# Performance work log

Hardware: AMD Instinct MI355X
Metric: run time of the kernel (lower is better)

## Reference

```python
import jax, jax.numpy as jnp
import numpy as np

N_NODES = 50000
N_EDGES = 600000
IN_FEAT = 128
OUT_FEAT = 128
NUM_RELS = 8


def setup_inputs() -> dict:
    key = jax.random.key(0)
    ks = jax.random.split(key, 8)
    h = jax.random.normal(ks[0], (N_NODES, IN_FEAT), dtype=jnp.float32)
    # xavier_uniform-like scale for relation weights
    limit = float(np.sqrt(6.0 / (IN_FEAT + OUT_FEAT)))
    weight = jax.random.uniform(ks[1], (NUM_RELS, IN_FEAT, OUT_FEAT), jnp.float32, -limit, limit)
    limit_g = float(np.sqrt(6.0 / (IN_FEAT + 1)))
    gate_weight = jax.random.uniform(ks[2], (NUM_RELS, IN_FEAT, 1), jnp.float32, -limit_g, limit_g)
    h_bias = jnp.zeros((OUT_FEAT,), jnp.float32)
    loop_weight = jax.random.uniform(ks[3], (IN_FEAT, OUT_FEAT), jnp.float32, -limit, limit)
    norm = jax.random.uniform(ks[4], (N_EDGES, 1), jnp.float32)
    src = jax.random.randint(ks[5], (N_EDGES,), 0, N_NODES, dtype=jnp.int32)
    dst = jax.random.randint(ks[6], (N_EDGES,), 0, N_NODES, dtype=jnp.int32)
    rel_type = jax.random.randint(ks[7], (N_EDGES,), 0, NUM_RELS, dtype=jnp.int32)
    return {"h": h, "weight": weight, "gate_weight": gate_weight, "h_bias": h_bias,
            "loop_weight": loop_weight, "norm": norm, "src": src, "dst": dst,
            "rel_type": rel_type}


def reference(h, weight, gate_weight, h_bias, loop_weight, norm, src, dst, rel_type):
    n_nodes = h.shape[0]
    # Transform all nodes under every relation once ([R, N, out]); cheaper than
    # materializing per-edge [E, in, out] weight gathers for small R.
    h_rel = jnp.einsum('ni,rio->rno', h, weight)          # [R, N, out]
    msg = h_rel[rel_type, src]                             # [E, out] gather
    msg = msg * norm                                       # per-edge norm
    # relation-specific scalar gate on src features
    gate_rel = jnp.einsum('ni,ri->rn', h, gate_weight[:, :, 0])  # [R, N]
    gate = jax.nn.sigmoid(gate_rel[rel_type, src])[:, None]      # [E, 1]
    msg = msg * gate
    # scatter-sum messages into destination nodes
    agg = jax.ops.segment_sum(msg, dst, num_segments=n_nodes)    # [N, out]
    out = agg + h_bias + h @ loop_weight                   # bias + self-loop
    out = jax.nn.relu(out)                                 # activation
    # dropout p=0.0 (deterministic) -> identity
    return out
```

## Files before the change

### kernel.cpp

```cpp
#include <hip/hip_runtime.h>

#define N_NODES 50000
#define N_EDGES 600000
#define F 128
#define NRELL 9
#define NB_SCAN 196
#define NB2 1563

#define WT3_OFF   0
#define H2_OFF    294912
#define GATE3_OFF 13094912
#define CNT3_OFF  14694912
#define EXCL3_OFF 16294912
#define BSUM3_OFF 17895168
#define REC3_OFF  17901568
#define A3_OFF    22701568
#define WS_NEED3  ((size_t)138012160)

#define GATE_OFF   294912
#define HREL_OFF   1894912
#define HREL_BYTES (9ll*N_NODES*128*2)
#define CNT_OFF    117094912
#define BASE_OFF   117294912
#define CUR_OFF    117494912
#define BSUM_OFF   117694912
#define SORT_OFF   117695936
#define WS_NEED2   ((size_t)120095936)
#define WS_NEED1   ((size_t)HREL_OFF + (size_t)HREL_BYTES)

typedef __attribute__((ext_vector_type(8))) short short8;
typedef __attribute__((ext_vector_type(4))) float floatx4;

__device__ inline unsigned short f32_to_bf16(float f) {
    unsigned u = __float_as_uint(f);
    unsigned r = u + 0x7fff + ((u >> 16) & 1);
    return (unsigned short)(r >> 16);
}
__device__ inline float bf16_to_f32(unsigned short s) {
    return __uint_as_float(((unsigned)s) << 16);
}
__device__ inline float bf16lo(unsigned m) { return __uint_as_float(m << 16); }
__device__ inline float bf16hi(unsigned m) { return __uint_as_float(m & 0xffff0000u); }
__device__ inline float sigmoidf(float x) { return 1.f / (1.f + __expf(-x)); }

__global__ void k_prep_w(const float* __restrict__ W, const float* __restrict__ LW,
                         unsigned short* __restrict__ Wt, int swz) {
    int idx = blockIdx.x * 256 + threadIdx.x;
    if (idx >= 9 * 128 * 128) return;
    int r = idx >> 14;
    int rem = idx & 16383;
    int i = rem >> 7, o = rem & 127;
    float v = (r < 8) ? W[(r << 14) + (i << 7) + o] : LW[(i << 7) + o];
    int pos;
    if (swz) {
        int g = (i >> 3) ^ (o & 7);
        pos = (r << 14) + (o << 7) + (g << 3) + (i & 7);
    } else {
        pos = (r << 14) + (o << 7) + i;
    }
    Wt[pos] = f32_to_bf16(v);
}

__global__ void k_prep_h(const float* __restrict__ h, const float* __restrict__ gw,
                         unsigned short* __restrict__ h2, float* __restrict__ gate) {
    int wave = threadIdx.x >> 6, lane = threadIdx.x & 63;
    int n = blockIdx.x * 4 + wave;
    float2 hv = *(const float2*)(h + (size_t)n * F + lane * 2);
    unsigned val = (unsigned)f32_to_bf16(hv.x) | ((unsigned)f32_to_bf16(hv.y) << 16);
    *(unsigned*)(h2 + (size_t)n * F + lane * 2) = val;
    #pragma unroll
    for (int r = 0; r < 8; ++r) {
        float2 wv = *(const float2*)(gw + r * F + lane * 2);
        float p = hv.x * wv.x + hv.y * wv.y;
        #pragma unroll
        for (int off = 32; off; off >>= 1) p += __shfl_xor(p, off);
        if (lane == 0) gate[r * N_NODES + n] = sigmoidf(p);
    }
}

__global__ void k_hist2(const int* __restrict__ dst, const int* __restrict__ rel,
                        int* __restrict__ cnt) {
    int e = blockIdx.x * 256 + threadIdx.x;
    if (e < N_EDGES) atomicAdd(&cnt[dst[e] * 8 + rel[e]], 1);
}

__global__ void k_s1(const int* __restrict__ cnt, int* __restrict__ excl,
                     int* __restrict__ bsum) {
    __shared__ int sh[256];
    int g = blockIdx.x * 256 + threadIdx.x;
    int v = (g < 400000) ? cnt[g] : 0;
    sh[threadIdx.x] = v;
    __syncthreads();
    #pragma unroll
    for (int off = 1; off < 256; off <<= 1) {
        int t = (threadIdx.x >= off) ? sh[threadIdx.x - off] : 0;
        __syncthreads();
        sh[threadIdx.x] += t;
        __syncthreads();
    }
    if (g < 400000) excl[g] = sh[threadIdx.x] - v;
    if (threadIdx.x == 255) bsum[blockIdx.x] = sh[255];
}

__global__ void k_s2(int* __restrict__ bsum) {
    __shared__ int sh[256];
    int t = threadIdx.x;
    int v[7];
    int s = 0;
    #pragma unroll
    for (int j = 0; j < 7; ++j) {
        int idx = t * 7 + j;
        v[j] = (idx < NB2) ? bsum[idx] : 0;
        s += v[j];
    }
    sh[t] = s;
    __syncthreads();
    #pragma unroll
    for (int off = 1; off < 256; off <<= 1) {
        int tt = (t >= off) ? sh[t - off] : 0;
        __syncthreads();
        sh[t] += tt;
        __syncthreads();
    }
    int run = sh[t] - s;
    #pragma unroll
    for (int j = 0; j < 7; ++j) {
        int idx = t * 7 + j;
        if (idx < NB2) bsum[idx] = run;
        run += v[j];
    }
}

__global__ void k_s3(int* __restrict__ excl, const int* __restrict__ bsum,
                     int* __restrict__ cursor) {
    int g = blockIdx.x * 256 + threadIdx.x;
    if (g < 400000) {
        int b = excl[g] + bsum[blockIdx.x];
        excl[g] = b;
        cursor[g] = b;
    }
    if (g == 0) excl[400000] = N_EDGES;
}

__global__ void k_scatter2(const int* __restrict__ src, const int* __restrict__ dst,
                           const int* __restrict__ rel, const float* __restrict__ norm,
                           const float* __restrict__ gate, int* __restrict__ cursor,
                           int2* __restrict__ rec) {
    int e = blockIdx.x * 256 + threadIdx.x;
    if (e >= N_EDGES) return;
    int d = dst[e], r = rel[e], s = src[e];
    int pos = atomicAdd(&cursor[d * 8 + r], 1);
    float sc = norm[e] * gate[r * N_NODES + s];
    rec[pos] = make_int2(s, __float_as_int(sc));
}

__global__ __launch_bounds__(256) void k_aggA(const unsigned short* __restrict__ h2,
                                              const int2* __restrict__ rec,
                                              const int* __restrict__ excl,
                                              unsigned short* __restrict__ A) {
    int wave = threadIdx.x >> 6, lane = threadIdx.x & 63;
    int n = blockIdx.x * 4 + wave;
    int ex = 0;
    if (lane < 9) ex = excl[n * 8 + lane];
    int e0 = __shfl(ex, 0), e8 = __shfl(ex, 8);
    int deg = e8 - e0;
    unsigned short* Arow = A + (size_t)n * 1152;
    int swo = (((lane >> 2) ^ (n & 7)) << 2) + (lane & 3);

    if (deg <= 64) {
        int rs = 0; float rsc = 0.f;
        if (lane < deg) {
            int2 rc = rec[e0 + lane];
            rs = rc.x; rsc = __int_as_float(rc.y);
        }
        for (int r = 0; r < 8; ++r) {
            int s = __shfl(ex, r) - e0;
            int e = __shfl(ex, r + 1) - e0;
            float a0 = 0.f, a1 = 0.f;
            for (int j = s; j < e; ++j) {
                int sj = __shfl(rs, j);
                float sc = __shfl(rsc, j);
                unsigned m = *(const unsigned*)(h2 + (size_t)sj * F + lane * 2);
                a0 += sc * bf16lo(m);
                a1 += sc * bf16hi(m);
            }
            unsigned val = (unsigned)f32_to_bf16(a0) | ((unsigned)f32_to_bf16(a1) << 16);
            ((unsigned*)(Arow + r * 128))[swo] = val;
        }
    } else {
        for (int r = 0; r < 8; ++r) {
            int s = __shfl(ex, r);
            int e = __shfl(ex, r + 1);
            float a0 = 0.f, a1 = 0.f;
            for (int idx = s; idx < e; ++idx) {
                int2 rc = rec[idx];
                float sc = __int_as_float(rc.y);
                unsigned m = *(const unsigned*)(h2 + (size_t)rc.x * F + lane * 2);
                a0 += sc * bf16lo(m);
                a1 += sc * bf16hi(m);
            }
            unsigned val = (unsigned)f32_to_bf16(a0) | ((unsigned)f32_to_bf16(a1) << 16);
            ((unsigned*)(Arow + r * 128))[swo] = val;
        }
    }
    unsigned hm = ((const unsigned*)(h2 + (size_t)n * F))[lane];
    ((unsigned*)(Arow + 8 * 128))[swo] = hm;
}

__global__ __launch_bounds__(256) void k_gemmA(const unsigned short* __restrict__ A,
                                               const unsigned short* __restrict__ Wt,
                                               const float* __restrict__ bias,
                                               float* __restrict__ out) {
    __shared__ unsigned short sA[16384];
    __shared__ unsigned short sB[16384];
    int tid = threadIdx.x;
    int nb = blockIdx.x * 128;
    int wave = tid >> 6, lane = tid & 63, lrow = lane & 15, quad = lane >> 4;

    floatx4 acc[2][8];
    #pragma unroll
    for (int mt = 0; mt < 2; ++mt)
        #pragma unroll
        for (int nt = 0; nt < 8; ++nt) acc[mt][nt] = (floatx4){0.f, 0.f, 0.f, 0.f};

    for (int kb = 0; kb < 9; ++kb) {
        __syncthreads();
        #pragma unroll
        for (int it = 0; it < 8; ++it) {
            int g = it * 256 + tid;
            int row = g >> 4, gr = g & 15;
            *(uint4*)(&sA[row * 128 + gr * 8]) =
                *(const uint4*)(A + (size_t)(nb + row) * 1152 + kb * 128 + gr * 8);
            *(uint4*)(&sB[row * 128 + gr * 8]) =
                *(const uint4*)(Wt + (kb << 14) + (g << 3));
        }
        __syncthreads();
        #pragma unroll
        for (int kt = 0; kt < 4; ++kt) {
            int j = kt * 4 + quad;
            int sw = (j ^ (lrow & 7)) << 3;
            short8 a0 = *(const short8*)(&sA[(wave * 32 + lrow) * 128 + sw]);
            short8 a1 = *(const short8*)(&sA[(wave * 32 + 16 + lrow) * 128 + sw]);
            #pragma unroll
            for (int nt = 0; nt < 8; ++nt) {
                short8 b = *(const short8*)(&sB[(nt * 16 + lrow) * 128 + sw]);
                acc[0][nt] = __builtin_amdgcn_mfma_f32_16x16x32_bf16(a0, b, acc[0][nt], 0, 0, 0);
                acc[1][nt] = __builtin_amdgcn_mfma_f32_16x16x32_bf16(a1, b, acc[1][nt], 0, 0, 0);
            }
        }
    }
    #pragma unroll
    for (int mt = 0; mt < 2; ++mt) {
        #pragma unroll
        for (int nt = 0; nt < 8; ++nt) {
            int col = nt * 16 + lrow;
            float bv = bias[col];
            #pragma unroll
            for (int g = 0; g < 4; ++g) {
                int row = nb + wave * 32 + mt * 16 + quad * 4 + g;
                if (row < N_NODES)
                    out[(size_t)row * F + col] = fmaxf(acc[mt][nt][g] + bv, 0.f);
            }
        }
    }
}

__global__ void k_gate(const float* __restrict__ h, const float* __restrict__ gw,
                       float* __restrict__ gate) {
    int wave = threadIdx.x >> 6, lane = threadIdx.x & 63;
    int n = blockIdx.x * 4 + wave;
    if (n >= N_NODES) return;
    float2 hv = *(const float2*)(h + (size_t)n * F + lane * 2);
    #pragma unroll
    for (int r = 0; r < 8; ++r) {
        float2 wv = *(const float2*)(gw + r * F + lane * 2);
        float p = hv.x * wv.x + hv.y * wv.y;
        #pragma unroll
        for (int off = 32; off; off >>= 1) p += __shfl_xor(p, off);
        if (lane == 0) gate[r * N_NODES + n] = sigmoidf(p);
    }
}

#define LDH 136
#define LDW 136
__global__ __launch_bounds__(256) void k_hrel(const float* __restrict__ h,
                                              const unsigned short* __restrict__ Wt,
                                              unsigned short* __restrict__ hrel) {
    __shared__ unsigned short hA[64 * LDH];
    __shared__ unsigned short wB[128 * LDW];
    int tid = threadIdx.x;
    int nb = blockIdx.x * 64;
    #pragma unroll
    for (int it = 0; it < 8; ++it) {
        int idx = it * 1024 + tid * 4;
        int row = idx >> 7, col = idx & 127;
        int node = nb + row;
        float4 v;
        if (node < N_NODES) v = *(const float4*)(h + (size_t)node * F + col);
        else                v = make_float4(0.f, 0.f, 0.f, 0.f);
        ushort4 b;
        b.x = f32_to_bf16(v.x); b.y = f32_to_bf16(v.y);
        b.z = f32_to_bf16(v.z); b.w = f32_to_bf16(v.w);
        *(ushort4*)(&hA[row * LDH + col]) = b;
    }
    int wave = tid >> 6, lane = tid & 63;
    int lrow = lane & 15, quad = lane >> 4;
    const unsigned short* aptr = &hA[(wave * 16 + lrow) * LDH + quad * 8];
    for (int r = 0; r < NRELL; ++r) {
        __syncthreads();
        #pragma unroll
        for (int it = 0; it < 8; ++it) {
            int idx = it * 2048 + tid * 8;
            int o = idx >> 7, i = idx & 127;
            *(uint4*)(&wB[o * LDW + i]) = *(const uint4*)(Wt + (r << 14) + idx);
        }
        __syncthreads();
        floatx4 acc[8];
        #pragma unroll
        for (int nt = 0; nt < 8; ++nt) acc[nt] = (floatx4){0.f, 0.f, 0.f, 0.f};
        #pragma unroll
        for (int kt = 0; kt < 4; ++kt) {
            short8 a = *(const short8*)(aptr + kt * 32);
            #pragma unroll
            for (int nt = 0; nt < 8; ++nt) {
                short8 b = *(const short8*)(&wB[(nt * 16 + lrow) * LDW + kt * 32 + quad * 8]);
                acc[nt] = __builtin_amdgcn_mfma_f32_16x16x32_bf16(a, b, acc[nt], 0, 0, 0);
            }
        }
        unsigned short* dstp = hrel + (size_t)r * N_NODES * F;
        #pragma unroll
        for (int nt = 0; nt < 8; ++nt) {
            #pragma unroll
            for (int g = 0; g < 4; ++g) {
                int node = nb + wave * 16 + quad * 4 + g;
                if (node < N_NODES)
                    dstp[(size_t)node * F + nt * 16 + lrow] = f32_to_bf16(acc[nt][g]);
            }
        }
    }
}

__global__ void k_hist(const int* __restrict__ dst, int* __restrict__ cnt) {
    int e = blockIdx.x * 256 + threadIdx.x;
    if (e < N_EDGES) atomicAdd(&cnt[dst[e]], 1);
}

__global__ void k_scan1(const int* __restrict__ cnt, int* __restrict__ excl,
                        int* __restrict__ bsum) {
    __shared__ int sh[256];
    int g = blockIdx.x * 256 + threadIdx.x;
    int v = (g < N_NODES) ? cnt[g] : 0;
    sh[threadIdx.x] = v;
    __syncthreads();
    #pragma unroll
    for (int off = 1; off < 256; off <<= 1) {
        int t = (threadIdx.x >= off) ? sh[threadIdx.x - off] : 0;
        __syncthreads();
        sh[threadIdx.x] += t;
        __syncthreads();
    }
    if (g < N_NODES) excl[g] = sh[threadIdx.x] - v;
    if (threadIdx.x == 255) bsum[blockIdx.x] = sh[255];
}

__global__ void k_scan2(int* __restrict__ bsum) {
    __shared__ int sh[256];
    int v = (threadIdx.x < NB_SCAN) ? bsum[threadIdx.x] : 0;
    sh[threadIdx.x] = v;
    __syncthreads();
    #pragma unroll
    for (int off = 1; off < 256; off <<= 1) {
        int t = (threadIdx.x >= off) ? sh[threadIdx.x - off] : 0;
        __syncthreads();
        sh[threadIdx.x] += t;
        __syncthreads();
    }
    if (threadIdx.x < NB_SCAN) bsum[threadIdx.x] = sh[threadIdx.x] - v;
}

__global__ void k_scan3(int* __restrict__ excl, const int* __restrict__ bsum,
                        int* __restrict__ cursor) {
    int g = blockIdx.x * 256 + threadIdx.x;
    if (g < N_NODES) {
        int b = excl[g] + bsum[blockIdx.x];
        excl[g] = b;
        cursor[g] = b;
    }
}

__global__ void k_scatter(const int* __restrict__ dst, int* __restrict__ cursor,
                          int* __restrict__ sorted) {
    int e = blockIdx.x * 256 + threadIdx.x;
    if (e < N_EDGES) {
        int pos = atomicAdd(&cursor[dst[e]], 1);
        sorted[pos] = e;
    }
}

__global__ __launch_bounds__(256) void k_agg(const unsigned short* __restrict__ hrel,
                      const float* __restrict__ gate,
                      const float* __restrict__ norm,
                      const int* __restrict__ src, const int* __restrict__ rel,
                      const int* __restrict__ sorted,
                      const int* __restrict__ base, const int* __restrict__ cnt,
                      const float* __restrict__ bias,
                      float* __restrict__ out) {
    int wave = threadIdx.x >> 6, lane = threadIdx.x & 63;
    int n = blockIdx.x * 4 + wave;
    if (n >= N_NODES) return;
    int startp = base[n];
    int deg = cnt[n];
    float acc0 = 0.f, acc1 = 0.f;
    for (int c0 = 0; c0 < deg; c0 += 64) {
        int myi = c0 + lane;
        float sc = 0.f;
        int row = 0;
        if (myi < deg) {
            int e = sorted[startp + myi];
            int s = src[e], r = rel[e];
            row = r * N_NODES + s;
            sc = norm[e] * gate[row];
        }
        int lim = (deg - c0 < 64) ? (deg - c0) : 64;
        for (int i = 0; i < lim; ++i) {
            float scl = __shfl(sc, i);
            int rw = __shfl(row, i);
            unsigned m = *(const unsigned*)(hrel + (size_t)rw * F + lane * 2);
            acc0 += scl * bf16lo(m);
            acc1 += scl * bf16hi(m);
        }
    }
    const unsigned short* hrel8 = hrel + (size_t)8 * N_NODES * F;
    unsigned l8 = *(const unsigned*)(hrel8 + (size_t)n * F + lane * 2);
    float2 bv = *(const float2*)(bias + lane * 2);
    float o0 = fmaxf(acc0 + bv.x + bf16lo(l8), 0.f);
    float o1 = fmaxf(acc1 + bv.y + bf16hi(l8), 0.f);
    *(float2*)(out + (size_t)n * F + lane * 2) = make_float2(o0, o1);
}

__global__ void k_edges(const unsigned short* __restrict__ hrel,
                        const float* __restrict__ gate,
                        const float* __restrict__ norm,
                        const int* __restrict__ src, const int* __restrict__ dst,
                        const int* __restrict__ rel,
                        float* __restrict__ out) {
    int wave = threadIdx.x >> 6, lane = threadIdx.x & 63;
    int e = blockIdx.x * 4 + wave;
    if (e >= N_EDGES) return;
    int s = src[e], d = dst[e], r = rel[e];
    float scale = norm[e] * gate[r * N_NODES + s];
    unsigned int m = *(const unsigned int*)(hrel + ((size_t)r * N_NODES + s) * F + lane * 2);
    float v0 = bf16lo(m) * scale;
    float v1 = bf16hi(m) * scale;
    float* op = out + (size_t)d * F + lane * 2;
    unsafeAtomicAdd(op, v0);
    unsafeAtomicAdd(op + 1, v1);
}

__global__ void k_final(float* __restrict__ out, const float* __restrict__ bias,
                        const unsigned short* __restrict__ hrel8) {
    int idx = blockIdx.x * 256 + threadIdx.x;
    if (idx >= N_NODES * 32) return;
    int node = idx >> 5, c4 = (idx & 31) * 4;
    float4 a = *(float4*)(out + (size_t)node * F + c4);
    float4 b = *(const float4*)(bias + c4);
    ushort4 l = *(const ushort4*)(hrel8 + (size_t)node * F + c4);
    float o0 = fmaxf(a.x + b.x + bf16_to_f32(l.x), 0.f);
    float o1 = fmaxf(a.y + b.y + bf16_to_f32(l.y), 0.f);
    float o2 = fmaxf(a.z + b.z + bf16_to_f32(l.z), 0.f);
    float o3 = fmaxf(a.w + b.w + bf16_to_f32(l.w), 0.f);
    *(float4*)(out + (size_t)node * F + c4) = make_float4(o0, o1, o2, o3);
}

__global__ void k_edges_fb(const float* __restrict__ h, const float* __restrict__ W,
                           const float* __restrict__ gw, const float* __restrict__ norm,
                           const int* __restrict__ src, const int* __restrict__ dst,
                           const int* __restrict__ rel, float* __restrict__ out) {
    int wave = threadIdx.x >> 6, lane = threadIdx.x & 63;
    int e = blockIdx.x * 4 + wave;
    if (e >= N_EDGES) return;
    int s = src[e], d = dst[e], r = rel[e];
    float2 hv = *(const float2*)(h + (size_t)s * F + lane * 2);
    float2 gv = *(const float2*)(gw + r * F + lane * 2);
    float p = hv.x * gv.x + hv.y * gv.y;
    #pragma unroll
    for (int off = 32; off; off >>= 1) p += __shfl_xor(p, off);
    float scale = norm[e] * sigmoidf(p);
    const float* wr = W + ((size_t)r << 14);
    float a0 = 0.f, a1 = 0.f;
    for (int i2 = 0; i2 < 64; ++i2) {
        float x0 = __shfl(hv.x, i2), x1 = __shfl(hv.y, i2);
        a0 += x0 * wr[(2 * i2) * F + lane]      + x1 * wr[(2 * i2 + 1) * F + lane];
        a1 += x0 * wr[(2 * i2) * F + 64 + lane] + x1 * wr[(2 * i2 + 1) * F + 64 + lane];
    }
    unsafeAtomicAdd(out + (size_t)d * F + lane,      a0 * scale);
    unsafeAtomicAdd(out + (size_t)d * F + 64 + lane, a1 * scale);
}

__global__ void k_final_fb(const float* __restrict__ h, const float* __restrict__ LW,
                           const float* __restrict__ bias, float* __restrict__ out) {
    int wave = threadIdx.x >> 6, lane = threadIdx.x & 63;
    int n = blockIdx.x * 4 + wave;
    if (n >= N_NODES) return;
    float2 hv = *(const float2*)(h + (size_t)n * F + lane * 2);
    float a0 = 0.f, a1 = 0.f;
    for (int i2 = 0; i2 < 64; ++i2) {
        float x0 = __shfl(hv.x, i2), x1 = __shfl(hv.y, i2);
        a0 += x0 * LW[(2 * i2) * F + lane]      + x1 * LW[(2 * i2 + 1) * F + lane];
        a1 += x0 * LW[(2 * i2) * F + 64 + lane] + x1 * LW[(2 * i2 + 1) * F + 64 + lane];
    }
    float* op = out + (size_t)n * F;
    op[lane]      = fmaxf(op[lane]      + bias[lane]      + a0, 0.f);
    op[64 + lane] = fmaxf(op[64 + lane] + bias[64 + lane] + a1, 0.f);
}

extern "C" void kernel_launch(void* const* d_in, const int* in_sizes, int n_in,
                              void* d_out, int out_size, void* d_ws, size_t ws_size,
                              hipStream_t stream) {
    const float* h    = (const float*)d_in[0];
    const float* W    = (const float*)d_in[1];
    const float* gw   = (const float*)d_in[2];
    const float* bias = (const float*)d_in[3];
    const float* lw   = (const float*)d_in[4];
    const float* norm = (const float*)d_in[5];
    const int* src    = (const int*)d_in[6];
    const int* dst    = (const int*)d_in[7];
    const int* rel    = (const int*)d_in[8];
    float* out = (float*)d_out;

    if (ws_size >= WS_NEED3) {
        unsigned short* Wt   = (unsigned short*)((char*)d_ws + WT3_OFF);
        unsigned short* h2   = (unsigned short*)((char*)d_ws + H2_OFF);
        float*          gate = (float*)((char*)d_ws + GATE3_OFF);
        int*            cnt  = (int*)((char*)d_ws + CNT3_OFF);
        int*            excl = (int*)((char*)d_ws + EXCL3_OFF);
        int*            bsum = (int*)((char*)d_ws + BSUM3_OFF);
        int2*           rec  = (int2*)((char*)d_ws + REC3_OFF);
        unsigned short* A    = (unsigned short*)((char*)d_ws + A3_OFF);

        hipMemsetAsync(cnt, 0, 400000 * sizeof(int), stream);
        k_prep_w<<<576, 256, 0, stream>>>(W, lw, Wt, 1);
        k_prep_h<<<12500, 256, 0, stream>>>(h, gw, h2, gate);
        k_hist2<<<2344, 256, 0, stream>>>(dst, rel, cnt);
        k_s1<<<NB2, 256, 0, stream>>>(cnt, excl, bsum);
        k_s2<<<1, 256, 0, stream>>>(bsum);
        k_s3<<<NB2, 256, 0, stream>>>(excl, bsum, cnt);
        k_scatter2<<<2344, 256, 0, stream>>>(src, dst, rel, norm, gate, cnt, rec);
        k_aggA<<<12500, 256, 0, stream>>>(h2, rec, excl, A);
        k_gemmA<<<391, 256, 0, stream>>>(A, Wt, bias, out);
    } else if (ws_size >= WS_NEED2) {
        unsigned short* Wt   = (unsigned short*)d_ws;
        float*          gate = (float*)((char*)d_ws + GATE_OFF);
        unsigned short* hrel = (unsigned short*)((char*)d_ws + HREL_OFF);
        int* cnt    = (int*)((char*)d_ws + CNT_OFF);
        int* base   = (int*)((char*)d_ws + BASE_OFF);
        int* cursor = (int*)((char*)d_ws + CUR_OFF);
        int* bsum   = (int*)((char*)d_ws + BSUM_OFF);
        int* sorted = (int*)((char*)d_ws + SORT_OFF);
        hipMemsetAsync(cnt, 0, N_NODES * sizeof(int), stream);
        k_prep_w<<<576, 256, 0, stream>>>(W, lw, Wt, 0);
        k_gate<<<12500, 256, 0, stream>>>(h, gw, gate);
        k_hist<<<2344, 256, 0, stream>>>(dst, cnt);
        k_scan1<<<NB_SCAN, 256, 0, stream>>>(cnt, base, bsum);
        k_scan2<<<1, 256, 0, stream>>>(bsum);
        k_scan3<<<NB_SCAN, 256, 0, stream>>>(base, bsum, cursor);
        k_scatter<<<2344, 256, 0, stream>>>(dst, cursor, sorted);
        k_hrel<<<782, 256, 0, stream>>>(h, Wt, hrel);
        k_agg<<<12500, 256, 0, stream>>>(hrel, gate, norm, src, rel, sorted,
                                         base, cnt, bias, out);
    } else if (ws_size >= WS_NEED1) {
        unsigned short* Wt   = (unsigned short*)d_ws;
        float*          gate = (float*)((char*)d_ws + GATE_OFF);
        unsigned short* hrel = (unsigned short*)((char*)d_ws + HREL_OFF);
        hipMemsetAsync(d_out, 0, (size_t)out_size * sizeof(float), stream);
        k_prep_w<<<576, 256, 0, stream>>>(W, lw, Wt, 0);
        k_gate<<<12500, 256, 0, stream>>>(h, gw, gate);
        k_hrel<<<782, 256, 0, stream>>>(h, Wt, hrel);
        k_edges<<<150000, 256, 0, stream>>>(hrel, gate, norm, src, dst, rel, out);
        k_final<<<6250, 256, 0, stream>>>(out, bias, hrel + (size_t)8 * N_NODES * F);
    } else {
        hipMemsetAsync(d_out, 0, (size_t)out_size * sizeof(float), stream);
        k_edges_fb<<<150000, 256, 0, stream>>>(h, W, gw, norm, src, dst, rel, out);
        k_final_fb<<<12500, 256, 0, stream>>>(h, lw, bias, out);
    }
}
```

Before: 272.0 us.

## Stream edges in aggregation with prefetch, read GEMM A-operand directly, double-buffer weights

The aggregation kernel now walks all edges of a node in one flat loop with a four-deep register prefetch of gathered source rows, instead of a separate loop per relation. The self-loop slab is no longer copied into the A buffer; the GEMM reads h2 directly for the last K block, so A shrinks to 1024 columns. The GEMM loads A fragments straight from global memory into registers, and streams weight tiles into a double-buffered LDS area with global_load_lds. This removes the A staging through LDS and one barrier per K step, at the cost of uncoalesced per-lane global reads of A and a single-barrier pipeline that depends on correct ordering.

```diff
diff --git a/kernel.cpp b/kernel.cpp
--- a/kernel.cpp
+++ b/kernel.cpp
@@ -15,7 +15,7 @@
 #define BSUM3_OFF 17895168
 #define REC3_OFF  17901568
 #define A3_OFF    22701568
-#define WS_NEED3  ((size_t)138012160)
+#define WS_NEED3  ((size_t)125199872)
 
 #define GATE_OFF   294912
 #define HREL_OFF   1894912
@@ -42,6 +42,12 @@
 __device__ inline float bf16lo(unsigned m) { return __uint_as_float(m << 16); }
 __device__ inline float bf16hi(unsigned m) { return __uint_as_float(m & 0xffff0000u); }
 __device__ inline float sigmoidf(float x) { return 1.f / (1.f + __expf(-x)); }
+
+__device__ __forceinline__ void gload_lds16(const void* gsrc, void* ldst) {
+    __builtin_amdgcn_global_load_lds(
+        (const __attribute__((address_space(1))) void*)gsrc,
+        (__attribute__((address_space(3))) void*)ldst, 16, 0, 0);
+}
 
 __global__ void k_prep_w(const float* __restrict__ W, const float* __restrict__ LW,
                          unsigned short* __restrict__ Wt, int swz) {
@@ -164,8 +170,7 @@
     if (lane < 9) ex = excl[n * 8 + lane];
     int e0 = __shfl(ex, 0), e8 = __shfl(ex, 8);
     int deg = e8 - e0;
-    unsigned short* Arow = A + (size_t)n * 1152;
-    int swo = (((lane >> 2) ^ (n & 7)) << 2) + (lane & 3);
+    unsigned* Arow = (unsigned*)(A + (size_t)n * 1024);
 
     if (deg <= 64) {
         int rs = 0; float rsc = 0.f;
@@ -173,19 +178,39 @@
             int2 rc = rec[e0 + lane];
             rs = rc.x; rsc = __int_as_float(rc.y);
         }
-        for (int r = 0; r < 8; ++r) {
-            int s = __shfl(ex, r) - e0;
-            int e = __shfl(ex, r + 1) - e0;
-            float a0 = 0.f, a1 = 0.f;
-            for (int j = s; j < e; ++j) {
-                int sj = __shfl(rs, j);
-                float sc = __shfl(rsc, j);
-                unsigned m = *(const unsigned*)(h2 + (size_t)sj * F + lane * 2);
-                a0 += sc * bf16lo(m);
-                a1 += sc * bf16hi(m);
-            }
+        unsigned m0 = 0, m1 = 0, m2 = 0, m3 = 0;
+        {
+            int s;
+            s = __shfl(rs, 0); if (0 < deg) m0 = *(const unsigned*)(h2 + (size_t)s * F + lane * 2);
+            s = __shfl(rs, 1); if (1 < deg) m1 = *(const unsigned*)(h2 + (size_t)s * F + lane * 2);
+            s = __shfl(rs, 2); if (2 < deg) m2 = *(const unsigned*)(h2 + (size_t)s * F + lane * 2);
+            s = __shfl(rs, 3); if (3 < deg) m3 = *(const unsigned*)(h2 + (size_t)s * F + lane * 2);
+        }
+        float a0 = 0.f, a1 = 0.f;
+        int r = 0;
+        int bnext = __shfl(ex, 1) - e0;
+        for (int j = 0; j < deg; ++j) {
+            while (j == bnext) {
+                unsigned val = (unsigned)f32_to_bf16(a0) | ((unsigned)f32_to_bf16(a1) << 16);
+                Arow[r * 64 + lane] = val;
+                a0 = 0.f; a1 = 0.f;
+                ++r;
+                bnext = __shfl(ex, r + 1) - e0;
+            }
+            float sc = __shfl(rsc, j);
+            a0 += sc * bf16lo(m0);
+            a1 += sc * bf16hi(m0);
+            m0 = m1; m1 = m2; m2 = m3;
+            int s4 = __shfl(rs, (j + 4) & 63);
+            unsigned mt = 0;
+            if (j + 4 < deg) mt = *(const unsigned*)(h2 + (size_t)s4 * F + lane * 2);
+            m3 = mt;
+        }
+        while (r < 8) {
             unsigned val = (unsigned)f32_to_bf16(a0) | ((unsigned)f32_to_bf16(a1) << 16);
-            ((unsigned*)(Arow + r * 128))[swo] = val;
+            Arow[r * 64 + lane] = val;
+            a0 = 0.f; a1 = 0.f;
+            ++r;
         }
     } else {
         for (int r = 0; r < 8; ++r) {
@@ -200,55 +225,76 @@
                 a1 += sc * bf16hi(m);
             }
             unsigned val = (unsigned)f32_to_bf16(a0) | ((unsigned)f32_to_bf16(a1) << 16);
-            ((unsigned*)(Arow + r * 128))[swo] = val;
-        }
-    }
-    unsigned hm = ((const unsigned*)(h2 + (size_t)n * F))[lane];
-    ((unsigned*)(Arow + 8 * 128))[swo] = hm;
+            Arow[r * 64 + lane] = val;
+        }
+    }
 }
 
 __global__ __launch_bounds__(256) void k_gemmA(const unsigned short* __restrict__ A,
+                                               const unsigned short* __restrict__ h2,
                                                const unsigned short* __restrict__ Wt,
                                                const float* __restrict__ bias,
                                                float* __restrict__ out) {
-    __shared__ unsigned short sA[16384];
-    __shared__ unsigned short sB[16384];
+    __shared__ unsigned short sB[2][16384];
     int tid = threadIdx.x;
     int nb = blockIdx.x * 128;
     int wave = tid >> 6, lane = tid & 63, lrow = lane & 15, quad = lane >> 4;
 
+    auto stageB = [&](int bufi, int kb2) {
+        #pragma unroll
+        for (int it = 0; it < 8; ++it) {
+            int c = it * 4 + wave;
+            gload_lds16((const char*)Wt + (kb2 << 15) + (c << 10) + lane * 16,
+                        (char*)(&sB[bufi][0]) + (c << 10));
+        }
+    };
+
     floatx4 acc[2][8];
     #pragma unroll
     for (int mt = 0; mt < 2; ++mt)
         #pragma unroll
         for (int nt = 0; nt < 8; ++nt) acc[mt][nt] = (floatx4){0.f, 0.f, 0.f, 0.f};
 
+    const unsigned short* Arow0 = A + (size_t)(nb + wave * 32 + lrow) * 1024;
+    const unsigned short* Arow1 = Arow0 + (size_t)16 * 1024;
+    const unsigned short* Hrow0 = h2 + (size_t)(nb + wave * 32 + lrow) * F;
+    const unsigned short* Hrow1 = Hrow0 + (size_t)16 * F;
+
+    stageB(0, 0);
+    __syncthreads();
+
     for (int kb = 0; kb < 9; ++kb) {
-        __syncthreads();
-        #pragma unroll
-        for (int it = 0; it < 8; ++it) {
-            int g = it * 256 + tid;
-            int row = g >> 4, gr = g & 15;
-            *(uint4*)(&sA[row * 128 + gr * 8]) =
-                *(const uint4*)(A + (size_t)(nb + row) * 1152 + kb * 128 + gr * 8);
-            *(uint4*)(&sB[row * 128 + gr * 8]) =
-                *(const uint4*)(Wt + (kb << 14) + (g << 3));
-        }
-        __syncthreads();
+        int buf = kb & 1;
+        short8 a0r[4], a1r[4];
+        if (kb < 8) {
+            #pragma unroll
+            for (int kt = 0; kt < 4; ++kt) {
+                int j = kt * 4 + quad;
+                a0r[kt] = *(const short8*)(Arow0 + kb * 128 + j * 8);
+                a1r[kt] = *(const short8*)(Arow1 + kb * 128 + j * 8);
+            }
+        } else {
+            #pragma unroll
+            for (int kt = 0; kt < 4; ++kt) {
+                int j = kt * 4 + quad;
+                a0r[kt] = *(const short8*)(Hrow0 + j * 8);
+                a1r[kt] = *(const short8*)(Hrow1 + j * 8);
+            }
+        }
+        if (kb < 8) stageB(buf ^ 1, kb + 1);
         #pragma unroll
         for (int kt = 0; kt < 4; ++kt) {
-            int j = kt * 4 + quad;
-            int sw = (j ^ (lrow & 7)) << 3;
-            short8 a0 = *(const short8*)(&sA[(wave * 32 + lrow) * 128 + sw]);
-            short8 a1 = *(const short8*)(&sA[(wave * 32 + 16 + lrow) * 128 + sw]);
+            int sw = ((kt * 4 + quad) ^ (lrow & 7)) << 3;
             #pragma unroll
             for (int nt = 0; nt < 8; ++nt) {
-                short8 b = *(const short8*)(&sB[(nt * 16 + lrow) * 128 + sw]);
-                acc[0][nt] = __builtin_amdgcn_mfma_f32_16x16x32_bf16(a0, b, acc[0][nt], 0, 0, 0);
-                acc[1][nt] = __builtin_amdgcn_mfma_f32_16x16x32_bf16(a1, b, acc[1][nt], 0, 0, 0);
-            }
-        }
-    }
+                short8 b = *(const short8*)(&sB[buf][(nt * 16 + lrow) * 128 + sw]);
+                acc[0][nt] = __builtin_amdgcn_mfma_f32_16x16x32_bf16(a0r[kt], b, acc[0][nt], 0, 0, 0);
+                acc[1][nt] = __builtin_amdgcn_mfma_f32_16x16x32_bf16(a1r[kt], b, acc[1][nt], 0, 0, 0);
+            }
+        }
+        __syncthreads();
+    }
+
     #pragma unroll
     for (int mt = 0; mt < 2; ++mt) {
         #pragma unroll
@@ -547,7 +593,7 @@
         k_s3<<<NB2, 256, 0, stream>>>(excl, bsum, cnt);
         k_scatter2<<<2344, 256, 0, stream>>>(src, dst, rel, norm, gate, cnt, rec);
         k_aggA<<<12500, 256, 0, stream>>>(h2, rec, excl, A);
-        k_gemmA<<<391, 256, 0, stream>>>(A, Wt, bias, out);
+        k_gemmA<<<391, 256, 0, stream>>>(A, h2, Wt, bias, out);
     } else if (ws_size >= WS_NEED2) {
         unsigned short* Wt   = (unsigned short*)d_ws;
         float*          gate = (float*)((char*)d_ws + GATE_OFF);
```

New measurement: 279.9 us. +2.9%, slower.

## Fuse per-relation aggregation and GEMM into one kernel via shared memory

Applied to the files above, without the earlier changes.

The separate aggregation kernel, which wrote a bf16 [N,1152] A matrix to global memory, and the GEMM kernel that read it back are replaced by a single 512-thread kernel. Each block aggregates 64 nodes' per-relation sums into padded, swizzled shared memory, keeps the transposed weights in registers, and runs MFMA directly on the shared tile. The goal is to remove the roughly 115 MB round trip of A and one launch. The gather loop also gains a 4-deep software prefetch of source rows. The costs are high register use (36 short8 fragments), lower occupancy from about 150 KB of shared memory per block, and aggregation and GEMM no longer overlapping across kernels.

```diff
diff --git a/kernel.cpp b/kernel.cpp
--- a/kernel.cpp
+++ b/kernel.cpp
@@ -14,8 +14,7 @@
 #define EXCL3_OFF 16294912
 #define BSUM3_OFF 17895168
 #define REC3_OFF  17901568
-#define A3_OFF    22701568
-#define WS_NEED3  ((size_t)138012160)
+#define WS_NEED3  ((size_t)22701568)
 
 #define GATE_OFF   294912
 #define HREL_OFF   1894912
@@ -28,6 +27,10 @@
 #define WS_NEED2   ((size_t)120095936)
 #define WS_NEED1   ((size_t)HREL_OFF + (size_t)HREL_BYTES)
 
+#define BMF 64
+#define GRIDF 782
+#define SAROW 1216
+
 typedef __attribute__((ext_vector_type(8))) short short8;
 typedef __attribute__((ext_vector_type(4))) float floatx4;
 
@@ -42,6 +45,9 @@
 __device__ inline float bf16lo(unsigned m) { return __uint_as_float(m << 16); }
 __device__ inline float bf16hi(unsigned m) { return __uint_as_float(m & 0xffff0000u); }
 __device__ inline float sigmoidf(float x) { return 1.f / (1.f + __expf(-x)); }
+__device__ inline unsigned packbf(float a0, float a1) {
+    return (unsigned)f32_to_bf16(a0) | ((unsigned)f32_to_bf16(a1) << 16);
+}
 
 __global__ void k_prep_w(const float* __restrict__ W, const float* __restrict__ LW,
                          unsigned short* __restrict__ Wt, int swz) {
@@ -66,7 +72,7 @@
     int wave = threadIdx.x >> 6, lane = threadIdx.x & 63;
     int n = blockIdx.x * 4 + wave;
     float2 hv = *(const float2*)(h + (size_t)n * F + lane * 2);
-    unsigned val = (unsigned)f32_to_bf16(hv.x) | ((unsigned)f32_to_bf16(hv.y) << 16);
+    unsigned val = packbf(hv.x, hv.y);
     *(unsigned*)(h2 + (size_t)n * F + lane * 2) = val;
     #pragma unroll
     for (int r = 0; r < 8; ++r) {
@@ -154,113 +160,133 @@
     rec[pos] = make_int2(s, __float_as_int(sc));
 }
 
-__global__ __launch_bounds__(256) void k_aggA(const unsigned short* __restrict__ h2,
-                                              const int2* __restrict__ rec,
-                                              const int* __restrict__ excl,
-                                              unsigned short* __restrict__ A) {
-    int wave = threadIdx.x >> 6, lane = threadIdx.x & 63;
-    int n = blockIdx.x * 4 + wave;
-    int ex = 0;
-    if (lane < 9) ex = excl[n * 8 + lane];
-    int e0 = __shfl(ex, 0), e8 = __shfl(ex, 8);
-    int deg = e8 - e0;
-    unsigned short* Arow = A + (size_t)n * 1152;
-    int swo = (((lane >> 2) ^ (n & 7)) << 2) + (lane & 3);
-
-    if (deg <= 64) {
-        int rs = 0; float rsc = 0.f;
-        if (lane < deg) {
-            int2 rc = rec[e0 + lane];
-            rs = rc.x; rsc = __int_as_float(rc.y);
-        }
-        for (int r = 0; r < 8; ++r) {
-            int s = __shfl(ex, r) - e0;
-            int e = __shfl(ex, r + 1) - e0;
-            float a0 = 0.f, a1 = 0.f;
-            for (int j = s; j < e; ++j) {
-                int sj = __shfl(rs, j);
-                float sc = __shfl(rsc, j);
-                unsigned m = *(const unsigned*)(h2 + (size_t)sj * F + lane * 2);
-                a0 += sc * bf16lo(m);
-                a1 += sc * bf16hi(m);
-            }
-            unsigned val = (unsigned)f32_to_bf16(a0) | ((unsigned)f32_to_bf16(a1) << 16);
-            ((unsigned*)(Arow + r * 128))[swo] = val;
-        }
-    } else {
-        for (int r = 0; r < 8; ++r) {
-            int s = __shfl(ex, r);
-            int e = __shfl(ex, r + 1);
-            float a0 = 0.f, a1 = 0.f;
-            for (int idx = s; idx < e; ++idx) {
-                int2 rc = rec[idx];
-                float sc = __int_as_float(rc.y);
-                unsigned m = *(const unsigned*)(h2 + (size_t)rc.x * F + lane * 2);
-                a0 += sc * bf16lo(m);
-                a1 += sc * bf16hi(m);
-            }
-            unsigned val = (unsigned)f32_to_bf16(a0) | ((unsigned)f32_to_bf16(a1) << 16);
-            ((unsigned*)(Arow + r * 128))[swo] = val;
-        }
-    }
-    unsigned hm = ((const unsigned*)(h2 + (size_t)n * F))[lane];
-    ((unsigned*)(Arow + 8 * 128))[swo] = hm;
-}
-
-__global__ __launch_bounds__(256) void k_gemmA(const unsigned short* __restrict__ A,
+__global__ __launch_bounds__(512) void k_fused(const unsigned short* __restrict__ h2,
+                                               const int2* __restrict__ rec,
+                                               const int* __restrict__ excl,
                                                const unsigned short* __restrict__ Wt,
                                                const float* __restrict__ bias,
                                                float* __restrict__ out) {
-    __shared__ unsigned short sA[16384];
-    __shared__ unsigned short sB[16384];
+    __shared__ unsigned short sAs[BMF * SAROW];
+    unsigned* sAu = (unsigned*)sAs;
     int tid = threadIdx.x;
-    int nb = blockIdx.x * 128;
-    int wave = tid >> 6, lane = tid & 63, lrow = lane & 15, quad = lane >> 4;
-
-    floatx4 acc[2][8];
-    #pragma unroll
-    for (int mt = 0; mt < 2; ++mt)
-        #pragma unroll
-        for (int nt = 0; nt < 8; ++nt) acc[mt][nt] = (floatx4){0.f, 0.f, 0.f, 0.f};
-
-    for (int kb = 0; kb < 9; ++kb) {
-        __syncthreads();
-        #pragma unroll
-        for (int it = 0; it < 8; ++it) {
-            int g = it * 256 + tid;
-            int row = g >> 4, gr = g & 15;
-            *(uint4*)(&sA[row * 128 + gr * 8]) =
-                *(const uint4*)(A + (size_t)(nb + row) * 1152 + kb * 128 + gr * 8);
-            *(uint4*)(&sB[row * 128 + gr * 8]) =
-                *(const uint4*)(Wt + (kb << 14) + (g << 3));
-        }
-        __syncthreads();
-        #pragma unroll
-        for (int kt = 0; kt < 4; ++kt) {
-            int j = kt * 4 + quad;
-            int sw = (j ^ (lrow & 7)) << 3;
-            short8 a0 = *(const short8*)(&sA[(wave * 32 + lrow) * 128 + sw]);
-            short8 a1 = *(const short8*)(&sA[(wave * 32 + 16 + lrow) * 128 + sw]);
-            #pragma unroll
-            for (int nt = 0; nt < 8; ++nt) {
-                short8 b = *(const short8*)(&sB[(nt * 16 + lrow) * 128 + sw]);
-                acc[0][nt] = __builtin_amdgcn_mfma_f32_16x16x32_bf16(a0, b, acc[0][nt], 0, 0, 0);
-                acc[1][nt] = __builtin_amdgcn_mfma_f32_16x16x32_bf16(a1, b, acc[1][nt], 0, 0, 0);
+    int wave = tid >> 6, lane = tid & 63;
+    int nb = blockIdx.x * BMF;
+    int n0 = nb + wave * 8;
+
+    int bin = n0 * 8 + lane;
+    int exa = excl[bin <= 400000 ? bin : 400000];
+    int b64 = (n0 + 8) * 8;
+    int e64s = excl[b64 <= 400000 ? b64 : 400000];
+
+    int rs[8]; float rscv[8];
+    #pragma unroll
+    for (int i = 0; i < 8; ++i) {
+        int e0 = __shfl(exa, i * 8);
+        int e8 = (i < 7) ? __shfl(exa, i * 8 + 8) : e64s;
+        int deg = e8 - e0;
+        rs[i] = 0; rscv[i] = 0.f;
+        if (deg <= 64 && lane < deg) {
+            int2 rc = rec[e0 + lane];
+            rs[i] = rc.x; rscv[i] = __int_as_float(rc.y);
+        }
+    }
+
+    #pragma unroll
+    for (int i = 0; i < 8; ++i) {
+        int e0 = __shfl(exa, i * 8);
+        int e8 = (i < 7) ? __shfl(exa, i * 8 + 8) : e64s;
+        int deg = e8 - e0;
+        int lr = wave * 8 + i;
+        unsigned* aw = sAu + lr * (SAROW / 2) + (((lane >> 2) ^ (lr & 7)) << 2) + (lane & 3);
+
+        if (deg <= 64) {
+            unsigned m0 = 0, m1 = 0, m2 = 0, m3 = 0;
+            {
+                int s;
+                s = __shfl(rs[i], 0); if (0 < deg) m0 = *(const unsigned*)(h2 + (size_t)s * F + lane * 2);
+                s = __shfl(rs[i], 1); if (1 < deg) m1 = *(const unsigned*)(h2 + (size_t)s * F + lane * 2);
+                s = __shfl(rs[i], 2); if (2 < deg) m2 = *(const unsigned*)(h2 + (size_t)s * F + lane * 2);
+                s = __shfl(rs[i], 3); if (3 < deg) m3 = *(const unsigned*)(h2 + (size_t)s * F + lane * 2);
             }
-        }
-    }
-    #pragma unroll
-    for (int mt = 0; mt < 2; ++mt) {
-        #pragma unroll
-        for (int nt = 0; nt < 8; ++nt) {
-            int col = nt * 16 + lrow;
-            float bv = bias[col];
-            #pragma unroll
-            for (int g = 0; g < 4; ++g) {
-                int row = nb + wave * 32 + mt * 16 + quad * 4 + g;
-                if (row < N_NODES)
-                    out[(size_t)row * F + col] = fmaxf(acc[mt][nt][g] + bv, 0.f);
+            float a0 = 0.f, a1 = 0.f;
+            int r = 0;
+            int bnext = ((i * 8 + 1 < 64) ? __shfl(exa, i * 8 + 1) : e64s) - e0;
+            for (int j = 0; j < deg; ++j) {
+                while (j == bnext) {
+                    aw[r * 64] = packbf(a0, a1);
+                    a0 = 0.f; a1 = 0.f;
+                    ++r;
+                    int idx = i * 8 + r + 1;
+                    bnext = ((idx < 64) ? __shfl(exa, idx) : e64s) - e0;
+                }
+                float sc = __shfl(rscv[i], j);
+                a0 += sc * bf16lo(m0);
+                a1 += sc * bf16hi(m0);
+                m0 = m1; m1 = m2; m2 = m3;
+                int s4 = __shfl(rs[i], (j + 4) & 63);
+                unsigned mt2 = 0;
+                if (j + 4 < deg) mt2 = *(const unsigned*)(h2 + (size_t)s4 * F + lane * 2);
+                m3 = mt2;
             }
+            while (r < 8) {
+                aw[r * 64] = packbf(a0, a1);
+                a0 = 0.f; a1 = 0.f;
+                ++r;
+            }
+        } else {
+            for (int r = 0; r < 8; ++r) {
+                int s = __shfl(exa, i * 8 + r);
+                int idx = i * 8 + r + 1;
+                int e = (idx < 64) ? __shfl(exa, idx) : e64s;
+                float a0 = 0.f, a1 = 0.f;
+                for (int p = s; p < e; ++p) {
+                    int2 rc = rec[p];
+                    float sc = __int_as_float(rc.y);
+                    unsigned m = *(const unsigned*)(h2 + (size_t)rc.x * F + lane * 2);
+                    a0 += sc * bf16lo(m);
+                    a1 += sc * bf16hi(m);
+                }
+                aw[r * 64] = packbf(a0, a1);
+            }
+        }
+        unsigned hm = 0;
+        int n = n0 + i;
+        if (n < N_NODES) hm = *(const unsigned*)(h2 + (size_t)n * F + lane * 2);
+        aw[512] = hm;
+    }
+
+    int lrow = lane & 15, quad = lane >> 4;
+    const unsigned short* bb = Wt + (size_t)(wave * 16 + lrow) * 128 + quad * 8;
+    short8 bf[36];
+    #pragma unroll
+    for (int ks = 0; ks < 36; ++ks)
+        bf[ks] = *(const short8*)(bb + ((ks >> 2) << 14) + (ks & 3) * 32);
+
+    __syncthreads();
+
+    floatx4 acc[4];
+    #pragma unroll
+    for (int mt = 0; mt < 4; ++mt) acc[mt] = (floatx4){0.f, 0.f, 0.f, 0.f};
+    #pragma unroll
+    for (int ks = 0; ks < 36; ++ks) {
+        int r = ks >> 2, kt = ks & 3;
+        int gsw = ((kt * 4 + quad) ^ (lrow & 7)) << 3;
+        #pragma unroll
+        for (int mt = 0; mt < 4; ++mt) {
+            short8 a = *(const short8*)(&sAs[(mt * 16 + lrow) * SAROW + r * 128 + gsw]);
+            acc[mt] = __builtin_amdgcn_mfma_f32_16x16x32_bf16(a, bf[ks], acc[mt], 0, 0, 0);
+        }
+    }
+
+    int col = wave * 16 + lrow;
+    float bv = bias[col];
+    #pragma unroll
+    for (int mt = 0; mt < 4; ++mt) {
+        #pragma unroll
+        for (int g = 0; g < 4; ++g) {
+            int row = nb + mt * 16 + quad * 4 + g;
+            if (row < N_NODES)
+                out[(size_t)row * F + col] = fmaxf(acc[mt][g] + bv, 0.f);
         }
     }
 }
@@ -536,18 +562,16 @@
         int*            excl = (int*)((char*)d_ws + EXCL3_OFF);
         int*            bsum = (int*)((char*)d_ws + BSUM3_OFF);
         int2*           rec  = (int2*)((char*)d_ws + REC3_OFF);
-        unsigned short* A    = (unsigned short*)((char*)d_ws + A3_OFF);
 
         hipMemsetAsync(cnt, 0, 400000 * sizeof(int), stream);
-        k_prep_w<<<576, 256, 0, stream>>>(W, lw, Wt, 1);
+        k_prep_w<<<576, 256, 0, stream>>>(W, lw, Wt, 0);
         k_prep_h<<<12500, 256, 0, stream>>>(h, gw, h2, gate);
         k_hist2<<<2344, 256, 0, stream>>>(dst, rel, cnt);
         k_s1<<<NB2, 256, 0, stream>>>(cnt, excl, bsum);
         k_s2<<<1, 256, 0, stream>>>(bsum);
         k_s3<<<NB2, 256, 0, stream>>>(excl, bsum, cnt);
         k_scatter2<<<2344, 256, 0, stream>>>(src, dst, rel, norm, gate, cnt, rec);
-        k_aggA<<<12500, 256, 0, stream>>>(h2, rec, excl, A);
-        k_gemmA<<<391, 256, 0, stream>>>(A, Wt, bias, out);
+        k_fused<<<GRIDF, 512, 0, stream>>>(h2, rec, excl, Wt, bias, out);
     } else if (ws_size >= WS_NEED2) {
         unsigned short* Wt   = (unsigned short*)d_ws;
         float*          gate = (float*)((char*)d_ws + GATE_OFF);
```

Result: slower. 402.5 us (+48.0%).

## Fuse preprocessing and sort pipeline into one cooperative persistent kernel

Applied to the files above, without the earlier changes.

Replaces the memset plus seven preprocessing launches (weight prep, h conversion/gate, histogram, three scan stages, scatter) with a single cooperative kernel that uses grid-wide syncs between phases, keeping the old launch sequence as a fallback if cooperative launch fails. The goal is to remove kernel launch gaps and per-launch tail effects across a chain of small kernels. In exchange it uses a fixed 1024-block persistent grid with grid.sync barriers, which may underuse bandwidth in some phases, and the single-block bsum scan still serializes.

```diff
diff --git a/kernel.cpp b/kernel.cpp
--- a/kernel.cpp
+++ b/kernel.cpp
@@ -1,4 +1,7 @@
 #include <hip/hip_runtime.h>
+#include <hip/hip_cooperative_groups.h>
+
+namespace cg = cooperative_groups;
 
 #define N_NODES 50000
 #define N_EDGES 600000
@@ -28,6 +31,8 @@
 #define WS_NEED2   ((size_t)120095936)
 #define WS_NEED1   ((size_t)HREL_OFF + (size_t)HREL_BYTES)
 
+#define PRE_GRID 1024
+
 typedef __attribute__((ext_vector_type(8))) short short8;
 typedef __attribute__((ext_vector_type(4))) float floatx4;
 
@@ -42,6 +47,120 @@
 __device__ inline float bf16lo(unsigned m) { return __uint_as_float(m << 16); }
 __device__ inline float bf16hi(unsigned m) { return __uint_as_float(m & 0xffff0000u); }
 __device__ inline float sigmoidf(float x) { return 1.f / (1.f + __expf(-x)); }
+__device__ inline unsigned packbf(float a0, float a1) {
+    return (unsigned)f32_to_bf16(a0) | ((unsigned)f32_to_bf16(a1) << 16);
+}
+
+__global__ __launch_bounds__(256) void k_pre(
+    const float* __restrict__ h, const float* __restrict__ W,
+    const float* __restrict__ gw, const float* __restrict__ lw,
+    const float* __restrict__ norm,
+    const int* __restrict__ src, const int* __restrict__ dst,
+    const int* __restrict__ rel,
+    unsigned short* __restrict__ Wt, unsigned short* __restrict__ h2,
+    float* __restrict__ gate, int* __restrict__ cnt,
+    int* __restrict__ excl, int* __restrict__ bsum, int2* __restrict__ rec)
+{
+    cg::grid_group grid = cg::this_grid();
+    __shared__ int sh[256];
+    int tid = threadIdx.x;
+    int nblk = gridDim.x;
+
+    for (int vb = blockIdx.x; vb < 13467; vb += nblk) {
+        if (vb < 391) {
+            int idx = vb * 1024 + tid * 4;
+            if (idx < 400000) *(int4*)(cnt + idx) = make_int4(0, 0, 0, 0);
+        } else if (vb < 967) {
+            int idx = (vb - 391) * 256 + tid;
+            int r = idx >> 14, rem = idx & 16383, i = rem >> 7, o = rem & 127;
+            float v = (r < 8) ? W[(r << 14) + (i << 7) + o] : lw[(i << 7) + o];
+            int g = (i >> 3) ^ (o & 7);
+            Wt[(r << 14) + (o << 7) + (g << 3) + (i & 7)] = f32_to_bf16(v);
+        } else {
+            int wave = tid >> 6, lane = tid & 63;
+            int n = (vb - 967) * 4 + wave;
+            float2 hv = *(const float2*)(h + (size_t)n * F + lane * 2);
+            *(unsigned*)(h2 + (size_t)n * F + lane * 2) = packbf(hv.x, hv.y);
+            #pragma unroll
+            for (int r = 0; r < 8; ++r) {
+                float2 wv = *(const float2*)(gw + r * F + lane * 2);
+                float p = hv.x * wv.x + hv.y * wv.y;
+                #pragma unroll
+                for (int off = 32; off; off >>= 1) p += __shfl_xor(p, off);
+                if (lane == 0) gate[r * N_NODES + n] = sigmoidf(p);
+            }
+        }
+    }
+    grid.sync();
+
+    for (int e = blockIdx.x * 256 + tid; e < N_EDGES; e += nblk * 256)
+        atomicAdd(&cnt[dst[e] * 8 + rel[e]], 1);
+    grid.sync();
+
+    for (int vb = blockIdx.x; vb < NB2; vb += nblk) {
+        int g = vb * 256 + tid;
+        int v = (g < 400000) ? cnt[g] : 0;
+        __syncthreads();
+        sh[tid] = v;
+        __syncthreads();
+        #pragma unroll
+        for (int off = 1; off < 256; off <<= 1) {
+            int t = (tid >= off) ? sh[tid - off] : 0;
+            __syncthreads();
+            sh[tid] += t;
+            __syncthreads();
+        }
+        if (g < 400000) excl[g] = sh[tid] - v;
+        if (tid == 255) bsum[vb] = sh[255];
+    }
+    grid.sync();
+
+    if (blockIdx.x == 0) {
+        int v[7]; int s = 0;
+        #pragma unroll
+        for (int j = 0; j < 7; ++j) {
+            int idx = tid * 7 + j;
+            v[j] = (idx < NB2) ? bsum[idx] : 0;
+            s += v[j];
+        }
+        __syncthreads();
+        sh[tid] = s;
+        __syncthreads();
+        #pragma unroll
+        for (int off = 1; off < 256; off <<= 1) {
+            int t = (tid >= off) ? sh[tid - off] : 0;
+            __syncthreads();
+            sh[tid] += t;
+            __syncthreads();
+        }
+        int run = sh[tid] - s;
+        #pragma unroll
+        for (int j = 0; j < 7; ++j) {
+            int idx = tid * 7 + j;
+            if (idx < NB2) bsum[idx] = run;
+            run += v[j];
+        }
+    }
+    grid.sync();
+
+    for (int vb = blockIdx.x; vb < NB2; vb += nblk) {
+        int g = vb * 256 + tid;
+        if (g < 400000) {
+            int b = excl[g] + bsum[vb];
+            excl[g] = b;
+            cnt[g] = b;
+        }
+    }
+    if (blockIdx.x == 0 && tid == 0) excl[400000] = N_EDGES;
+    grid.sync();
+
+    for (int e = blockIdx.x * 256 + tid; e < N_EDGES; e += nblk * 256) {
+        int d = dst[e], r = rel[e], s = src[e];
+        int pos = atomicAdd(&cnt[d * 8 + r], 1);
+        float sc = norm[e] * gate[r * N_NODES + s];
+        rec[pos] = make_int2(s, __float_as_int(sc));
+    }
+}
 
 __global__ void k_prep_w(const float* __restrict__ W, const float* __restrict__ LW,
                          unsigned short* __restrict__ Wt, int swz) {
@@ -66,7 +185,7 @@
     int wave = threadIdx.x >> 6, lane = threadIdx.x & 63;
     int n = blockIdx.x * 4 + wave;
     float2 hv = *(const float2*)(h + (size_t)n * F + lane * 2);
-    unsigned val = (unsigned)f32_to_bf16(hv.x) | ((unsigned)f32_to_bf16(hv.y) << 16);
+    unsigned val = packbf(hv.x, hv.y);
     *(unsigned*)(h2 + (size_t)n * F + lane * 2) = val;
     #pragma unroll
     for (int r = 0; r < 8; ++r) {
@@ -184,8 +303,7 @@
                 a0 += sc * bf16lo(m);
                 a1 += sc * bf16hi(m);
             }
-            unsigned val = (unsigned)f32_to_bf16(a0) | ((unsigned)f32_to_bf16(a1) << 16);
-            ((unsigned*)(Arow + r * 128))[swo] = val;
+            ((unsigned*)(Arow + r * 128))[swo] = packbf(a0, a1);
         }
     } else {
         for (int r = 0; r < 8; ++r) {
@@ -199,8 +317,7 @@
                 a0 += sc * bf16lo(m);
                 a1 += sc * bf16hi(m);
             }
-            unsigned val = (unsigned)f32_to_bf16(a0) | ((unsigned)f32_to_bf16(a1) << 16);
-            ((unsigned*)(Arow + r * 128))[swo] = val;
+            ((unsigned*)(Arow + r * 128))[swo] = packbf(a0, a1);
         }
     }
     unsigned hm = ((const unsigned*)(h2 + (size_t)n * F))[lane];
@@ -538,14 +655,23 @@
         int2*           rec  = (int2*)((char*)d_ws + REC3_OFF);
         unsigned short* A    = (unsigned short*)((char*)d_ws + A3_OFF);
 
-        hipMemsetAsync(cnt, 0, 400000 * sizeof(int), stream);
-        k_prep_w<<<576, 256, 0, stream>>>(W, lw, Wt, 1);
-        k_prep_h<<<12500, 256, 0, stream>>>(h, gw, h2, gate);
-        k_hist2<<<2344, 256, 0, stream>>>(dst, rel, cnt);
-        k_s1<<<NB2, 256, 0, stream>>>(cnt, excl, bsum);
-        k_s2<<<1, 256, 0, stream>>>(bsum);
-        k_s3<<<NB2, 256, 0, stream>>>(excl, bsum, cnt);
-        k_scatter2<<<2344, 256, 0, stream>>>(src, dst, rel, norm, gate, cnt, rec);
+        void* kargs[] = {(void*)&h, (void*)&W, (void*)&gw, (void*)&lw, (void*)&norm,
+                         (void*)&src, (void*)&dst, (void*)&rel,
+                         (void*)&Wt, (void*)&h2, (void*)&gate, (void*)&cnt,
+                         (void*)&excl, (void*)&bsum, (void*)&rec};
+        hipError_t ce = hipLaunchCooperativeKernel(
+            reinterpret_cast<const void*>(k_pre), dim3(PRE_GRID), dim3(256),
+            kargs, 0, stream);
+        if (ce != hipSuccess) {
+            hipMemsetAsync(cnt, 0, 400000 * sizeof(int), stream);
+            k_prep_w<<<576, 256, 0, stream>>>(W, lw, Wt, 1);
+            k_prep_h<<<12500, 256, 0, stream>>>(h, gw, h2, gate);
+            k_hist2<<<2344, 256, 0, stream>>>(dst, rel, cnt);
+            k_s1<<<NB2, 256, 0, stream>>>(cnt, excl, bsum);
+            k_s2<<<1, 256, 0, stream>>>(bsum);
+            k_s3<<<NB2, 256, 0, stream>>>(excl, bsum, cnt);
+            k_scatter2<<<2344, 256, 0, stream>>>(src, dst, rel, norm, gate, cnt, rec);
+        }
         k_aggA<<<12500, 256, 0, stream>>>(h2, rec, excl, A);
         k_gemmA<<<391, 256, 0, stream>>>(A, Wt, bias, out);
     } else if (ws_size >= WS_NEED2) {
```

Measured after the change: 829.3 us. 205% more time.
